# Performance work log

Measured on AMD Instinct MI355X. Metric: run time of the kernel, lower is better.

## Reference

```python
import jax, jax.numpy as jnp
import numpy as np

MODES = 32
NUM_BLOCKS = 4
NUM_EXPERTS = 16
TOP_K = 4
TEMPERATURE = 2.0


def _gelu(t):
    return jax.nn.gelu(t, approximate=False)  # torch F.gelu default (erf)


def _c1(x, w, b):
    # 1x1 conv: x [B,C,H,W], w [O,C], b [O]
    return jnp.einsum('bchw,oc->bohw', x, w) + b[None, :, None, None]


def _group_norm(x, w, b, groups=8, eps=1e-5):
    B, C, H, W = x.shape
    xg = x.reshape(B, groups, C // groups, H, W)
    mu = xg.mean(axis=(2, 3, 4), keepdims=True)
    var = xg.var(axis=(2, 3, 4), keepdims=True)
    xn = ((xg - mu) * jax.lax.rsqrt(var + eps)).reshape(B, C, H, W)
    return xn * w[None, :, None, None] + b[None, :, None, None]


def _bn_eval(x, g, b, rm, rv, eps=1e-5):
    # eval-mode BatchNorm with running stats
    return (x - rm) * jax.lax.rsqrt(rv + eps) * g + b


def _afno(x, w1, b1, w2, b2):
    # x: [B,C,H,W] (channel_first). Block-diagonal complex MLP on low FFT modes.
    B, C, H, W = x.shape
    bs = C // NUM_BLOCKS
    xp = x.transpose(0, 2, 3, 1)                      # [B,H,W,C]
    xf = jnp.fft.rfft2(xp, axes=(1, 2), norm='ortho') # [B,H,Wf,C] complex64
    Wf = xf.shape[2]
    xf = xf.reshape(B, H, Wf, NUM_BLOCKS, bs)
    m = MODES
    xm = xf[:, :m, :m]                                # kept modes only
    xr, xi = xm.real, xm.imag
    o1r = _gelu(jnp.einsum('bhwni,nio->bhwno', xr, w1[0])
                - jnp.einsum('bhwni,nio->bhwno', xi, w1[1]) + b1[0])
    o1i = _gelu(jnp.einsum('bhwni,nio->bhwno', xi, w1[0])
                + jnp.einsum('bhwni,nio->bhwno', xr, w1[1]) + b1[1])
    o2r = (jnp.einsum('bhwni,nio->bhwno', o1r, w2[0])
           - jnp.einsum('bhwni,nio->bhwno', o1i, w2[1]) + b2[0])
    o2i = (jnp.einsum('bhwni,nio->bhwno', o1i, w2[0])
           + jnp.einsum('bhwni,nio->bhwno', o1r, w2[1]) + b2[1])
    of = jnp.zeros((B, H, Wf, NUM_BLOCKS, bs), dtype=xf.dtype)
    of = of.at[:, :m, :m].set(o2r + 1j * o2i)
    out = jnp.fft.irfft2(of.reshape(B, H, Wf, C), s=(H, W), axes=(1, 2), norm='ortho')
    out = out + xp
    return out.transpose(0, 3, 1, 2)


def _forward(x, gn1_w, gn1_b, afno_w1, afno_b1, afno_w2, afno_b2,
             gn2_w, gn2_b, fe_w, fe_b, g1_w, g1_b, bn1_g, bn1_b, bn1_rm, bn1_rv,
             ca_w1, ca_b1, ca_w2, ca_b2, g2_w, g2_b, bn2_g, bn2_b, bn2_rm, bn2_rv,
             g3_w, g3_b, shared_w, shared_b, expert_w, expert_b):
    residual = x
    h = _group_norm(x, gn1_w, gn1_b)
    h = _afno(h, afno_w1, afno_b1, afno_w2, afno_b2)
    h = h + residual            # double_skip
    residual = h
    h = _group_norm(h, gn2_w, gn2_b)
    # MoEImage (eval mode -> loss_gate = 0)
    feats = _gelu(_c1(h, fe_w, fe_b))
    shared = jnp.zeros_like(h)
    for s in range(shared_w.shape[0]):
        shared = shared + _gelu(_c1(feats, shared_w[s], shared_b[s])) / shared_w.shape[0]
    # gating on global-avg-pooled features (1x1 convs == linears)
    gf = feats.mean(axis=(2, 3))                              # [B,C]
    h1 = _gelu(_bn_eval(gf @ g1_w.T + g1_b, bn1_g, bn1_b, bn1_rm, bn1_rv))
    a = _gelu(h1 @ ca_w1.T + ca_b1) @ ca_w2.T + ca_b2
    h1 = h1 * jax.nn.sigmoid(2.0 * a)                          # avg==max pool on 1x1 map
    h2 = _gelu(_bn_eval(h1 @ g2_w.T + g2_b, bn2_g, bn2_b, bn2_rm, bn2_rv))
    scores = h2 @ g3_w.T + g3_b                                # [B,E]
    vals, idx = jax.lax.top_k(scores, TOP_K)
    wts = jax.nn.softmax(vals / TEMPERATURE, axis=1)
    B = x.shape[0]
    gate_w = jnp.zeros((B, NUM_EXPERTS), x.dtype).at[jnp.arange(B)[:, None], idx].add(wts)
    out = shared
    for e in range(NUM_EXPERTS):
        out = out + _gelu(_c1(feats, expert_w[e], expert_b[e])) * gate_w[:, e][:, None, None, None]
    return out + residual


def setup_inputs():
    key = jax.random.key(0)
    ks = jax.random.split(key, 16)
    B, C, H, W = 8, 64, 192, 192
    nb = NUM_BLOCKS
    bs = C // nb
    E = NUM_EXPERTS
    scale = 1.0 / (bs * bs)
    f32 = jnp.float32
    n = lambda k, shape: jax.random.normal(k, shape, f32) * 0.02
    return {
        'x': jax.random.normal(ks[0], (B, C, H, W), f32),
        'gn1_w': jnp.ones((C,), f32), 'gn1_b': jnp.zeros((C,), f32),
        'afno_w1': jax.random.uniform(ks[1], (2, nb, bs, bs), f32) * scale,
        'afno_b1': jax.random.uniform(ks[2], (2, nb, bs), f32) * scale,
        'afno_w2': jax.random.uniform(ks[3], (2, nb, bs, bs), f32) * scale,
        'afno_b2': jax.random.uniform(ks[4], (2, nb, bs), f32) * scale,
        'gn2_w': jnp.ones((C,), f32), 'gn2_b': jnp.zeros((C,), f32),
        'fe_w': n(ks[5], (C, C)), 'fe_b': jnp.zeros((C,), f32),
        'g1_w': n(ks[6], (2 * C, C)), 'g1_b': jnp.zeros((2 * C,), f32),
        'bn1_g': jnp.ones((2 * C,), f32), 'bn1_b': jnp.zeros((2 * C,), f32),
        'bn1_rm': jnp.zeros((2 * C,), f32), 'bn1_rv': jnp.ones((2 * C,), f32),
        'ca_w1': n(ks[7], (2 * C // 16, 2 * C)), 'ca_b1': jnp.zeros((2 * C // 16,), f32),
        'ca_w2': n(ks[8], (2 * C, 2 * C // 16)), 'ca_b2': jnp.zeros((2 * C,), f32),
        'g2_w': n(ks[9], (C, 2 * C)), 'g2_b': jnp.zeros((C,), f32),
        'bn2_g': jnp.ones((C,), f32), 'bn2_b': jnp.zeros((C,), f32),
        'bn2_rm': jnp.zeros((C,), f32), 'bn2_rv': jnp.ones((C,), f32),
        'g3_w': n(ks[10], (E, C)), 'g3_b': jnp.zeros((E,), f32),
        'shared_w': n(ks[11], (2, C, C)), 'shared_b': jnp.zeros((2, C), f32),
        'expert_w': n(ks[12], (E, C, C)), 'expert_b': jnp.zeros((E, C), f32),
    }


def reference(x, gn1_w, gn1_b, afno_w1, afno_b1, afno_w2, afno_b2,
              gn2_w, gn2_b, fe_w, fe_b, g1_w, g1_b, bn1_g, bn1_b, bn1_rm, bn1_rv,
              ca_w1, ca_b1, ca_w2, ca_b2, g2_w, g2_b, bn2_g, bn2_b, bn2_rm, bn2_rv,
              g3_w, g3_b, shared_w, shared_b, expert_w, expert_b):
    return _forward(x, gn1_w, gn1_b, afno_w1, afno_b1, afno_w2, afno_b2,
                    gn2_w, gn2_b, fe_w, fe_b, g1_w, g1_b, bn1_g, bn1_b, bn1_rm, bn1_rv,
                    ca_w1, ca_b1, ca_w2, ca_b2, g2_w, g2_b, bn2_g, bn2_b, bn2_rm, bn2_rv,
                    g3_w, g3_b, shared_w, shared_b, expert_w, expert_b)
```

## Files before the change

kernel.cpp:

```cpp
#include <hip/hip_runtime.h>
#include <math.h>

#define TPI 6.283185307179586f

typedef __attribute__((ext_vector_type(8))) short bf8v;
typedef __attribute__((ext_vector_type(4))) float f4v;

#define MFMA(a,b,c) __builtin_amdgcn_mfma_f32_16x16x32_bf16((a),(b),(c),0,0,0)

__device__ __forceinline__ float gelu_f(float v){
  return 0.5f*v*(1.0f+erff(v*0.7071067811865475f));
}
__device__ __forceinline__ float gelu_fast(float x){
  float x2=x*x;
  float inner=fmaf(0.044715f*x2, x, x);
  float e=__expf(1.5957691216057308f*inner);
  float r=__builtin_amdgcn_rcpf(1.0f+e);
  return fmaf(-x, r, x);
}
__device__ __forceinline__ float gelu_sig(float x){
  float e=__expf(-1.702f*x);
  return x*__builtin_amdgcn_rcpf(1.0f+e);
}
__device__ __forceinline__ unsigned short f2b(float f){
  union{float f; unsigned u;} v; v.f=f;
  unsigned r=v.u + 0x7FFFu + ((v.u>>16)&1u);
  return (unsigned short)(r>>16);
}

__global__ __launch_bounds__(256) void prep(const float* __restrict__ shw, const float* __restrict__ exw,
    const float* __restrict__ shb, const float* __restrict__ exb, const float* __restrict__ few,
    unsigned short* __restrict__ T, unsigned short* __restrict__ wall, float* __restrict__ ball,
    unsigned short* __restrict__ wfe, float* __restrict__ gfp){
  const float a = TPI/192.0f;
  int stride=gridDim.x*256;
  for(int i=blockIdx.x*256+threadIdx.x; i<61440; i+=stride){
    float v;
    if(i<12288){
      int n1=i/192, w=i%192; int kw=n1>>1, c=n1&1;
      int m=(kw*w)%192; float cs,sn; sincosf((float)m*a,&sn,&cs);
      v = c ? -sn : cs;
    } else if(i<36864){
      int j=i-12288; int n1=j/384, k1=j%384; int kh=n1>>1, d=n1&1; int h=k1>>1, c=k1&1;
      int m=(kh*h)%192; float cs,sn; sincosf((float)m*a,&sn,&cs);
      float e = d ? (c ? cs : -sn) : (c ? sn : cs);
      v = e*(1.0f/192.0f);
    } else if(i<49152){
      int j=i-36864; int h=j/64, k1=j%64; int kh=k1>>1, c=k1&1;
      int m=(h*kh)%192; float cs,sn; sincosf((float)m*a,&sn,&cs);
      v = c ? sn : cs;
    } else {
      int j=i-49152; int w=j/64, k1=j%64; int kw=k1>>1, d=k1&1;
      float f = kw ? (2.0f/192.0f) : (1.0f/192.0f);
      int m=(w*kw)%192; float cs,sn; sincosf((float)m*a,&sn,&cs);
      v = d ? -f*sn : f*cs;
    }
    T[i]=f2b(v);
  }
  for(int i=blockIdx.x*256+threadIdx.x;i<73728;i+=stride) wall[i]=f2b(i<8192?shw[i]:exw[i-8192]);
  for(int i=blockIdx.x*256+threadIdx.x;i<1152;i+=stride)  ball[i]=(i<128)?shb[i]:exb[i-128];
  for(int i=blockIdx.x*256+threadIdx.x;i<4096;i+=stride)  wfe[i]=f2b(few[i]);
  for(int i=blockIdx.x*256+threadIdx.x;i<512;i+=stride)   gfp[i]=0.f;
}

__global__ void gn_finalize(const float* __restrict__ part, const float* __restrict__ gw,
                            const float* __restrict__ gb, float2* __restrict__ sb){
  int g=threadIdx.x; if(g>=64) return;
  float S=0,SS=0;
  for(int j=0;j<8;j++){ S+=part[(g*8+j)*2]; SS+=part[(g*8+j)*2+1]; }
  const float inv=1.0f/294912.0f;
  float mean=S*inv, var=SS*inv-mean*mean;
  float rstd=rsqrtf(var+1e-5f);
  int b=g>>3, gg=g&7;
  for(int k=0;k<8;k++){
    int c=gg*8+k;
    float sc=rstd*gw[c];
    sb[b*64+c]=make_float2(sc, gb[c]-mean*sc);
  }
}

__global__ __launch_bounds__(256) void fwd_dft(const float* __restrict__ x,
      const unsigned short* __restrict__ TBf1, const unsigned short* __restrict__ TBf2,
      float* __restrict__ Xm2, float* __restrict__ part1){
  __shared__ __align__(16) unsigned short ldsA[64*200];
  __shared__ __align__(16) float sX[2048];
  __shared__ float red[8];
  int t=threadIdx.x, bc=blockIdx.x;
  int wave=t>>6, l=t&63, lr=l&15, lg=l>>4;
  const float* xch = x + (size_t)bc*36864;
  for(int i=t;i<1536;i+=256){
    int row=i/24, chunk=i%24;
    *(uint4*)&ldsA[row*200 + chunk*8] = *(const uint4*)(TBf1 + row*192 + chunk*8);
  }
  __syncthreads();
  float s_=0.f, ss_=0.f;
  f4v acc1[3][4];
  for(int mt=0;mt<3;mt++){
    int m0=(wave+mt*4)*16;
    const float* xrow = xch + (m0+lr)*192 + lg*8;
    bf8v af[6];
    #pragma unroll
    for(int ks=0;ks<6;ks++){
      float4 u0=*(const float4*)(xrow+ks*32);
      float4 u1=*(const float4*)(xrow+ks*32+4);
      s_ += u0.x+u0.y+u0.z+u0.w+u1.x+u1.y+u1.z+u1.w;
      ss_+= u0.x*u0.x+u0.y*u0.y+u0.z*u0.z+u0.w*u0.w
           +u1.x*u1.x+u1.y*u1.y+u1.z*u1.z+u1.w*u1.w;
      bf8v a;
      a[0]=(short)f2b(u0.x); a[1]=(short)f2b(u0.y); a[2]=(short)f2b(u0.z); a[3]=(short)f2b(u0.w);
      a[4]=(short)f2b(u1.x); a[5]=(short)f2b(u1.y); a[6]=(short)f2b(u1.z); a[7]=(short)f2b(u1.w);
      af[ks]=a;
    }
    #pragma unroll
    for(int nt=0;nt<4;nt++){
      f4v acc={0.f,0.f,0.f,0.f};
      #pragma unroll
      for(int ks=0;ks<6;ks++){
        bf8v b=*(const bf8v*)&ldsA[(nt*16+lr)*200 + ks*32 + lg*8];
        acc=MFMA(af[ks],b,acc);
      }
      acc1[mt][nt]=acc;
    }
  }
  __syncthreads();
  for(int mt=0;mt<3;mt++){
    int m0=(wave+mt*4)*16;
    #pragma unroll
    for(int nt=0;nt<4;nt++){
      int n1=nt*16+lr; int kw=n1>>1, c=n1&1;
      #pragma unroll
      for(int reg=0;reg<4;reg++){
        int h=m0+4*lg+reg;
        ldsA[kw*392 + 2*h + c]=f2b(acc1[mt][nt][reg]);
      }
    }
  }
  __syncthreads();
  for(int pp=0;pp<2;pp++){
    int p=wave+pp*4;
    int m0=(p>>2)*16, n0=(p&3)*16;
    f4v acc={0.f,0.f,0.f,0.f};
    #pragma unroll
    for(int ks=0;ks<12;ks++){
      bf8v a=*(const bf8v*)&ldsA[(m0+lr)*392 + ks*32 + lg*8];
      bf8v b=*(const bf8v*)(TBf2 + (n0+lr)*384 + ks*32 + lg*8);
      acc=MFMA(a,b,acc);
    }
    int n1=n0+lr; int kh=n1>>1, d=n1&1;
    #pragma unroll
    for(int reg=0;reg<4;reg++){
      int kw=m0+4*lg+reg;
      sX[(kh*32+kw)*2 + d]=acc[reg];
    }
  }
  __syncthreads();
  float* dst=Xm2+(size_t)bc*2048;
  for(int i=t;i<512;i+=256) *(float4*)(dst+i*4)=*(const float4*)(sX+i*4);
  #pragma unroll
  for(int o=32;o>0;o>>=1){ s_+=__shfl_down(s_,o); ss_+=__shfl_down(ss_,o); }
  if(l==0){ red[wave]=s_; red[4+wave]=ss_; }
  __syncthreads();
  if(t==0){
    part1[bc*2]  =red[0]+red[1]+red[2]+red[3];
    part1[bc*2+1]=red[4]+red[5]+red[6]+red[7];
  }
}

__global__ __launch_bounds__(256) void mode_mlp(const float* __restrict__ Xm2, const float2* __restrict__ sb1,
    const float* __restrict__ w1, const float* __restrict__ b1,
    const float* __restrict__ w2, const float* __restrict__ b2,
    float* __restrict__ S2){
  __shared__ float w10[1024], w11[1024], w20[1024], w21[1024];
  __shared__ float b10[64], b11[64], b20[64], b21[64];
  __shared__ float2 sbl[64];
  __shared__ float xr[32][64], xi[32][64];
  __shared__ float o1r[32][64], o1i[32][64];
  int t=threadIdx.x;
  int b=blockIdx.x>>5, kh=blockIdx.x&31;
  for(int i=t;i<1024;i+=256){ w10[i]=w1[i]; w11[i]=w1[1024+i]; w20[i]=w2[i]; w21[i]=w2[1024+i]; }
  if(t<64){ b10[t]=b1[t]; b11[t]=b1[64+t]; b20[t]=b2[t]; b21[t]=b2[64+t]; sbl[t]=sb1[b*64+t]; }
  __syncthreads();
  for(int q=0;q<16;q++){
    int idx=q*256+t; int c=idx>>6, jj=idx&63;
    float2 s=sbl[c];
    float v=Xm2[((size_t)(b*64+c))*2048 + kh*64 + jj]*s.x;
    if(kh==0 && jj==0) v += 192.0f*s.y;
    if(jj&1) xi[jj>>1][c]=v; else xr[jj>>1][c]=v;
  }
  __syncthreads();
  int tl=t&63, n=tl>>4, o=tl&15, wb=n*256+o;
  #pragma unroll
  for(int it=0;it<8;it++){
    int kw=(t>>6)+it*4;
    float a_r=b10[tl], a_i=b11[tl];
    #pragma unroll
    for(int i=0;i<16;i++){
      float rr=xr[kw][n*16+i], im=xi[kw][n*16+i];
      float W0=w10[wb+i*16], W1=w11[wb+i*16];
      a_r=fmaf(rr,W0,fmaf(-im,W1,a_r));
      a_i=fmaf(im,W0,fmaf( rr,W1,a_i));
    }
    o1r[kw][tl]=gelu_f(a_r); o1i[kw][tl]=gelu_f(a_i);
  }
  __syncthreads();
  #pragma unroll
  for(int it=0;it<8;it++){
    int kw=(t>>6)+it*4;
    float c_r=b20[tl], c_i=b21[tl];
    #pragma unroll
    for(int i=0;i<16;i++){
      float rr=o1r[kw][n*16+i], im=o1i[kw][n*16+i];
      float W0=w20[wb+i*16], W1=w21[wb+i*16];
      c_r=fmaf(rr,W0,fmaf(-im,W1,c_r));
      c_i=fmaf(im,W0,fmaf( rr,W1,c_i));
    }
    xr[kw][tl]=c_r; xi[kw][tl]=c_i;
  }
  __syncthreads();
  for(int q=0;q<16;q++){
    int idx=q*256+t; int c=idx>>6, jj=idx&63;
    float v = (jj&1) ? xi[jj>>1][c] : xr[jj>>1][c];
    S2[((size_t)(b*64+c))*2048 + kh*64 + jj]=v;
  }
}

__global__ __launch_bounds__(256) void inv_dft(const float* __restrict__ S2,
      const unsigned short* __restrict__ TAi, const unsigned short* __restrict__ TBi,
      const float* __restrict__ x, const float2* __restrict__ sb,
      float* __restrict__ h2, float* __restrict__ part2){
  __shared__ __align__(16) unsigned short Bs[64*72];
  __shared__ __align__(16) unsigned short GL[192*72];
  __shared__ float red[8];
  int t=threadIdx.x, bc=blockIdx.x;
  int wave=t>>6, l=t&63, lr=l&15, lg=l>>4;
  const float* sp=S2+(size_t)bc*2048;
  for(int i=t;i<1024;i+=256){
    int kh=i>>5, kw=i&31;
    float Sr=sp[(kh*32+kw)*2], Si=sp[(kh*32+kw)*2+1];
    unsigned short br=f2b(Sr), bi_=f2b(Si), nbi=f2b(-Si);
    Bs[(2*kw+0)*72 + 2*kh+0]=br;
    Bs[(2*kw+0)*72 + 2*kh+1]=nbi;
    Bs[(2*kw+1)*72 + 2*kh+0]=bi_;
    Bs[(2*kw+1)*72 + 2*kh+1]=br;
  }
  __syncthreads();
  for(int mt=0;mt<3;mt++){
    int m0=(wave+mt*4)*16;
    bf8v a0=*(const bf8v*)(TAi + (m0+lr)*64 + lg*8);
    bf8v a1=*(const bf8v*)(TAi + (m0+lr)*64 + 32 + lg*8);
    #pragma unroll
    for(int nt=0;nt<4;nt++){
      f4v acc={0.f,0.f,0.f,0.f};
      bf8v b0=*(const bf8v*)&Bs[(nt*16+lr)*72 + lg*8];
      bf8v b1=*(const bf8v*)&Bs[(nt*16+lr)*72 + 32 + lg*8];
      acc=MFMA(a0,b0,acc); acc=MFMA(a1,b1,acc);
      #pragma unroll
      for(int reg=0;reg<4;reg++)
        GL[(m0+4*lg+reg)*72 + nt*16+lr]=f2b(acc[reg]);
    }
  }
  __syncthreads();
  float2 sv=sb[bc];
  float cA=sv.x+1.0f, cB=sv.y;
  asm volatile("" : "+v"(cA), "+v"(cB));
  const float* xch=x+(size_t)bc*36864;
  float* och=h2+(size_t)bc*36864;
  float s_=0.f, ss_=0.f;
  for(int mt=0;mt<3;mt++){
    int m0=(wave+mt*4)*16;
    bf8v a0=*(const bf8v*)&GL[(m0+lr)*72 + lg*8];
    bf8v a1=*(const bf8v*)&GL[(m0+lr)*72 + 32 + lg*8];
    for(int nt=0;nt<12;nt++){
      int n0=nt*16;
      f4v acc={0.f,0.f,0.f,0.f};
      bf8v b0=*(const bf8v*)(TBi + (n0+lr)*64 + lg*8);
      bf8v b1=*(const bf8v*)(TBi + (n0+lr)*64 + 32 + lg*8);
      acc=MFMA(a0,b0,acc); acc=MFMA(a1,b1,acc);
      int w=n0+lr;
      #pragma unroll
      for(int reg=0;reg<4;reg++){
        int h=m0+4*lg+reg;
        int ga=h*192+w;
        float xv=xch[ga];
        float val=acc[reg]+fmaf(cA,xv,cB);
        och[ga]=val;
        s_+=val; ss_+=val*val;
      }
    }
  }
  #pragma unroll
  for(int o=32;o>0;o>>=1){ s_+=__shfl_down(s_,o); ss_+=__shfl_down(ss_,o); }
  if(l==0){ red[wave]=s_; red[4+wave]=ss_; }
  __syncthreads();
  if(t==0){
    part2[bc*2]  =red[0]+red[1]+red[2]+red[3];
    part2[bc*2+1]=red[4]+red[5]+red[6]+red[7];
  }
}

__global__ __launch_bounds__(256,4) void gf_k(const float* __restrict__ h2, const float2* __restrict__ sb,
    const unsigned short* __restrict__ wfe, const float* __restrict__ feb,
    float* __restrict__ gfp, unsigned short* __restrict__ feats){
  __shared__ __align__(16) unsigned short A[128*72];
  __shared__ float sgf[64];
  int t=threadIdx.x;
  int blk=blockIdx.x, b=blk/288, tile=blk-b*288, hw0=tile*128;
  if(t<64) sgf[t]=0.f;
  float4 v[8];
  #pragma unroll
  for(int k=0;k<8;k++){
    int i=t+k*256; int c=i>>5, q=i&31;
    v[k]=*(const float4*)&h2[(size_t)(b*64+c)*36864 + hw0 + q*4];
  }
  #pragma unroll
  for(int k=0;k<8;k++){
    int i=t+k*256; int c=i>>5, q=i&31;
    float2 s=sb[b*64+c];
    int px0=q*4, sw=((px0>>4)&3)<<3, cc=c^sw;
    A[(px0+0)*72+cc]=f2b(fmaf(v[k].x,s.x,s.y));
    A[(px0+1)*72+cc]=f2b(fmaf(v[k].y,s.x,s.y));
    A[(px0+2)*72+cc]=f2b(fmaf(v[k].z,s.x,s.y));
    A[(px0+3)*72+cc]=f2b(fmaf(v[k].w,s.x,s.y));
  }
  __syncthreads();
  int wave=t>>6, l=t&63, lr=l&15, lg=l>>4;
  int pxb=wave*32;
  bf8v af[2][2];
  #pragma unroll
  for(int fm=0;fm<2;fm++){
    int row=pxb+fm*16+lr, sw=((row>>4)&3)<<3;
    #pragma unroll
    for(int ks=0;ks<2;ks++) af[fm][ks]=*(const bf8v*)&A[row*72+((ks*32+lg*8)^sw)];
  }
  float gsum[4]={0.f,0.f,0.f,0.f};
  #pragma unroll
  for(int fn=0;fn<4;fn++){
    bf8v b0=*(const bf8v*)(wfe+(fn*16+lr)*64+lg*8);
    bf8v b1=*(const bf8v*)(wfe+(fn*16+lr)*64+32+lg*8);
    float bs=feb[fn*16+lr];
    #pragma unroll
    for(int fm=0;fm<2;fm++){
      f4v acc={0.f,0.f,0.f,0.f};
      acc=MFMA(af[fm][0],b0,acc);
      acc=MFMA(af[fm][1],b1,acc);
      int swm=(((pxb+fm*16)>>4)&3)<<3;
      int cc=(fn*16+lr)^swm;
      #pragma unroll
      for(int r=0;r<4;r++){
        float g=gelu_fast(acc[r]+bs);
        gsum[fn]+=g;
        A[(pxb+fm*16+4*lg+r)*72+cc]=f2b(g);
      }
    }
  }
  #pragma unroll
  for(int fn=0;fn<4;fn++){
    float v2=gsum[fn];
    v2+=__shfl_xor(v2,16); v2+=__shfl_xor(v2,32);
    if(lg==0) atomicAdd(&sgf[fn*16+lr], v2);
  }
  __syncthreads();
  if(t<64) atomicAdd(&gfp[b*64+t], sgf[t]);
  #pragma unroll
  for(int k=0;k<4;k++){
    int i=t+k*256; int px=i>>3, c0=(i&7)*8, sw=((px>>4)&3)<<3;
    *(uint4*)&feats[(size_t)(b*36864+hw0+px)*64+c0] = *(const uint4*)&A[px*72+(c0^sw)];
  }
}

__global__ __launch_bounds__(128) void gating(const float* __restrict__ gfp,
  const float* __restrict__ g1w, const float* __restrict__ g1b,
  const float* __restrict__ bn1g, const float* __restrict__ bn1b, const float* __restrict__ bn1m, const float* __restrict__ bn1v,
  const float* __restrict__ cw1, const float* __restrict__ cb1, const float* __restrict__ cw2, const float* __restrict__ cb2,
  const float* __restrict__ g2w, const float* __restrict__ g2b,
  const float* __restrict__ bn2g, const float* __restrict__ bn2b, const float* __restrict__ bn2m, const float* __restrict__ bn2v,
  const float* __restrict__ g3w, const float* __restrict__ g3b, float2* __restrict__ act){
  __shared__ float gf[8][64];
  __shared__ float h1[8][128];
  __shared__ float a1[8][8];
  __shared__ float h2g[8][64];
  __shared__ float sc[8][16];
  int t=threadIdx.x;
  for(int i=t;i<512;i+=128) gf[i>>6][i&63]=gfp[i]*(1.0f/36864.0f);
  __syncthreads();
  for(int i=t;i<1024;i+=128){
    int b=i>>7, j=i&127;
    float s=g1b[j];
    for(int c=0;c<64;c++) s=fmaf(gf[b][c], g1w[j*64+c], s);
    s=(s-bn1m[j])*rsqrtf(bn1v[j]+1e-5f)*bn1g[j]+bn1b[j];
    h1[b][j]=gelu_f(s);
  }
  __syncthreads();
  if(t<64){
    int b=t>>3, k=t&7; float s=cb1[k];
    for(int j=0;j<128;j++) s=fmaf(h1[b][j], cw1[k*128+j], s);
    a1[b][k]=gelu_f(s);
  }
  __syncthreads();
  for(int i=t;i<1024;i+=128){
    int b=i>>7, j=i&127;
    float s=cb2[j];
    for(int k=0;k<8;k++) s=fmaf(a1[b][k], cw2[j*8+k], s);
    h1[b][j]=h1[b][j]/(1.0f+expf(-2.0f*s));
  }
  __syncthreads();
  for(int i=t;i<512;i+=128){
    int b=i>>6, j=i&63;
    float s=g2b[j];
    for(int k=0;k<128;k++) s=fmaf(h1[b][k], g2w[j*128+k], s);
    s=(s-bn2m[j])*rsqrtf(bn2v[j]+1e-5f)*bn2g[j]+bn2b[j];
    h2g[b][j]=gelu_f(s);
  }
  __syncthreads();
  {
    int b=t>>4, e=t&15;
    float s=g3b[e];
    for(int c=0;c<64;c++) s=fmaf(h2g[b][c], g3w[e*64+c], s);
    sc[b][e]=s;
  }
  __syncthreads();
  if(t<8){
    int b=t;
    float v[16];
    for(int e=0;e<16;e++) v[e]=sc[b][e];
    float vals[4]; int idx[4];
    for(int k=0;k<4;k++){
      float best=-1e30f; int bi=0;
      for(int e=0;e<16;e++) if(v[e]>best){best=v[e];bi=e;}
      vals[k]=best; idx[k]=bi; v[bi]=-1e30f;
    }
    float m=vals[0], ssum=0.f, w[4];
    for(int k=0;k<4;k++){ w[k]=expf((vals[k]-m)*0.5f); ssum+=w[k]; }
    act[b*6+0]=make_float2(0.5f, __int_as_float(0));
    act[b*6+1]=make_float2(0.5f, __int_as_float(1));
    for(int k=0;k<4;k++) act[b*6+2+k]=make_float2(w[k]/ssum, __int_as_float(2+idx[k]));
  }
}

__global__ __launch_bounds__(256,4) void final_k(const unsigned short* __restrict__ feats,
  const float* __restrict__ h2w,
  const unsigned short* __restrict__ wall, const float* __restrict__ ball,
  const float2* __restrict__ act, float* __restrict__ out){
  __shared__ __align__(16) float Fo[32*132];
  int t=threadIdx.x;
  int blk=blockIdx.x, b=blk/288, tile=blk-b*288, hw0=tile*128;
  int wave=t>>6, l=t&63, lr=l&15, lg=l>>4;
  int pxb=wave*32;
  float gv[6]; int tv[6];
  #pragma unroll
  for(int j=0;j<6;j++){
    float2 aw=act[b*6+j];
    gv[j]=aw.x; tv[j]=__float_as_int(aw.y);
  }
  const unsigned short* fbase = feats + (size_t)(b*36864+hw0)*64;
  bf8v af2[2][2];
  #pragma unroll
  for(int fm=0;fm<2;fm++){
    int row=pxb+fm*16+lr;
    #pragma unroll
    for(int ks=0;ks<2;ks++)
      af2[fm][ks]=*(const bf8v*)(fbase + (size_t)row*64 + ks*32 + lg*8);
  }
  #pragma unroll
  for(int half=0;half<2;half++){
    float oa[2][2][4]={};
    #pragma unroll
    for(int j=0;j<6;j++){
      float g=gv[j];
      const unsigned short* wp=wall+tv[j]*4096;
      const float* bp=ball+tv[j]*64;
      #pragma unroll
      for(int fn2=0;fn2<2;fn2++){
        int fn=half*2+fn2;
        bf8v b0=*(const bf8v*)(wp+(fn*16+lr)*64+lg*8);
        bf8v b1=*(const bf8v*)(wp+(fn*16+lr)*64+32+lg*8);
        float bs=bp[fn*16+lr];
        #pragma unroll
        for(int fm=0;fm<2;fm++){
          f4v acc={0.f,0.f,0.f,0.f};
          acc=MFMA(af2[fm][0],b0,acc);
          acc=MFMA(af2[fm][1],b1,acc);
          #pragma unroll
          for(int r=0;r<4;r++)
            oa[fm][fn2][r]=fmaf(g, gelu_sig(acc[r]+bs), oa[fm][fn2][r]);
        }
      }
    }
    __syncthreads();
    #pragma unroll
    for(int fm=0;fm<2;fm++)
      #pragma unroll
      for(int fn2=0;fn2<2;fn2++){
        int ocl=fn2*16+lr;
        *(float4*)&Fo[ocl*132 + pxb + fm*16 + 4*lg] =
            make_float4(oa[fm][fn2][0],oa[fm][fn2][1],oa[fm][fn2][2],oa[fm][fn2][3]);
      }
    __syncthreads();
    for(int i=t;i<1024;i+=256){
      int ocl=i>>5, px0=(i&31)*4;
      int oc=half*32+ocl;
      size_t base=(size_t)(b*64+oc)*36864 + hw0 + px0;
      float4 rv=*(const float4*)&h2w[base];
      float4 ov=*(const float4*)&Fo[ocl*132+px0];
      *(float4*)&out[base]=make_float4(ov.x+rv.x,ov.y+rv.y,ov.z+rv.z,ov.w+rv.w);
    }
  }
}

extern "C" void kernel_launch(void* const* d_in, const int* in_sizes, int n_in,
                              void* d_out, int out_size, void* d_ws, size_t ws_size,
                              hipStream_t stream){
  const float* x    =(const float*)d_in[0];
  const float* gn1w =(const float*)d_in[1];
  const float* gn1b =(const float*)d_in[2];
  const float* aw1  =(const float*)d_in[3];
  const float* ab1  =(const float*)d_in[4];
  const float* aw2  =(const float*)d_in[5];
  const float* ab2  =(const float*)d_in[6];
  const float* gn2w =(const float*)d_in[7];
  const float* gn2b =(const float*)d_in[8];
  const float* few  =(const float*)d_in[9];
  const float* feb  =(const float*)d_in[10];
  const float* g1w  =(const float*)d_in[11];
  const float* g1b  =(const float*)d_in[12];
  const float* bn1g =(const float*)d_in[13];
  const float* bn1b =(const float*)d_in[14];
  const float* bn1m =(const float*)d_in[15];
  const float* bn1v =(const float*)d_in[16];
  const float* cw1  =(const float*)d_in[17];
  const float* cb1  =(const float*)d_in[18];
  const float* cw2  =(const float*)d_in[19];
  const float* cb2  =(const float*)d_in[20];
  const float* g2w  =(const float*)d_in[21];
  const float* g2b  =(const float*)d_in[22];
  const float* bn2g =(const float*)d_in[23];
  const float* bn2b =(const float*)d_in[24];
  const float* bn2m =(const float*)d_in[25];
  const float* bn2v =(const float*)d_in[26];
  const float* g3w  =(const float*)d_in[27];
  const float* g3b  =(const float*)d_in[28];
  const float* shw  =(const float*)d_in[29];
  const float* shb  =(const float*)d_in[30];
  const float* exw  =(const float*)d_in[31];
  const float* exb  =(const float*)d_in[32];

  float* out=(float*)d_out;
  float* ws=(float*)d_ws;

  float*  part1 = ws;
  float*  part2 = ws+1024;
  float2* sb1   = (float2*)(ws+2048);
  float2* sb2   = (float2*)(ws+3072);
  float2* act   = (float2*)(ws+4096);
  float*  gfp   = ws+4224;
  float*  Xm2   = ws+8192;
  float*  S2    = ws+1056768;
  unsigned short* Tbl  = (unsigned short*)(ws+2105344);
  unsigned short* wall = (unsigned short*)(ws+2136064);
  float*          ball = ws+2172928;
  unsigned short* wfe  = (unsigned short*)(ws+2174080);
  unsigned short* feats= (unsigned short*)(ws+2176128);
  float*  h2w   = ws+11613312;
  const unsigned short* TBf1 = Tbl;
  const unsigned short* TBf2 = Tbl+12288;
  const unsigned short* TAi  = Tbl+36864;
  const unsigned short* TBi  = Tbl+49152;

  prep<<<64,256,0,stream>>>(shw, exw, shb, exb, few, Tbl, wall, ball, wfe, gfp);
  fwd_dft <<<512,256,0,stream>>>(x, TBf1, TBf2, Xm2, part1);
  gn_finalize<<<1,64,0,stream>>>(part1, gn1w, gn1b, sb1);
  mode_mlp<<<256,256,0,stream>>>(Xm2, sb1, aw1, ab1, aw2, ab2, S2);
  inv_dft <<<512,256,0,stream>>>(S2, TAi, TBi, x, sb1, h2w, part2);
  gn_finalize<<<1,64,0,stream>>>(part2, gn2w, gn2b, sb2);
  gf_k<<<2304,256,0,stream>>>(h2w, sb2, wfe, feb, gfp, feats);
  gating <<<1,128,0,stream>>>(gfp, g1w,g1b, bn1g,bn1b,bn1m,bn1v,
                              cw1,cb1,cw2,cb2, g2w,g2b, bn2g,bn2b,bn2m,bn2v,
                              g3w,g3b, act);
  final_k<<<2304,256,0,stream>>>(feats, h2w, wall, ball, act, out);
}
```

Before: 211.2 us.

## Store intermediate h2 in bf16 and write final output directly from registers

The AFNO output h2 is now stored as bf16 instead of fp32. That halves its write traffic in inv_dft and its read traffic in gf_k and final_k. final_k also drops its shared-memory staging tile and two barriers, adding the residual and writing float4 output straight from the MFMA accumulators. The cost is lower precision on the residual path added to the output, and less coalesced 16-byte stores in final_k.

```diff
diff --git a/kernel.cpp b/kernel.cpp
--- a/kernel.cpp
+++ b/kernel.cpp
@@ -26,6 +26,9 @@
   union{float f; unsigned u;} v; v.f=f;
   unsigned r=v.u + 0x7FFFu + ((v.u>>16)&1u);
   return (unsigned short)(r>>16);
+}
+__device__ __forceinline__ float b2f(unsigned short h){
+  union{unsigned u; float f;} v; v.u=((unsigned)h)<<16; return v.f;
 }
 
 __global__ __launch_bounds__(256) void prep(const float* __restrict__ shw, const float* __restrict__ exw,
@@ -227,7 +230,7 @@
 __global__ __launch_bounds__(256) void inv_dft(const float* __restrict__ S2,
       const unsigned short* __restrict__ TAi, const unsigned short* __restrict__ TBi,
       const float* __restrict__ x, const float2* __restrict__ sb,
-      float* __restrict__ h2, float* __restrict__ part2){
+      unsigned short* __restrict__ h2b, float* __restrict__ part2){
   __shared__ __align__(16) unsigned short Bs[64*72];
   __shared__ __align__(16) unsigned short GL[192*72];
   __shared__ float red[8];
@@ -264,7 +267,7 @@
   float cA=sv.x+1.0f, cB=sv.y;
   asm volatile("" : "+v"(cA), "+v"(cB));
   const float* xch=x+(size_t)bc*36864;
-  float* och=h2+(size_t)bc*36864;
+  unsigned short* och=h2b+(size_t)bc*36864;
   float s_=0.f, ss_=0.f;
   for(int mt=0;mt<3;mt++){
     int m0=(wave+mt*4)*16;
@@ -283,7 +286,7 @@
         int ga=h*192+w;
         float xv=xch[ga];
         float val=acc[reg]+fmaf(cA,xv,cB);
-        och[ga]=val;
+        och[ga]=f2b(val);
         s_+=val; ss_+=val*val;
       }
     }
@@ -298,7 +301,7 @@
   }
 }
 
-__global__ __launch_bounds__(256,4) void gf_k(const float* __restrict__ h2, const float2* __restrict__ sb,
+__global__ __launch_bounds__(256,4) void gf_k(const unsigned short* __restrict__ h2b, const float2* __restrict__ sb,
     const unsigned short* __restrict__ wfe, const float* __restrict__ feb,
     float* __restrict__ gfp, unsigned short* __restrict__ feats){
   __shared__ __align__(16) unsigned short A[128*72];
@@ -306,21 +309,21 @@
   int t=threadIdx.x;
   int blk=blockIdx.x, b=blk/288, tile=blk-b*288, hw0=tile*128;
   if(t<64) sgf[t]=0.f;
-  float4 v[8];
-  #pragma unroll
-  for(int k=0;k<8;k++){
-    int i=t+k*256; int c=i>>5, q=i&31;
-    v[k]=*(const float4*)&h2[(size_t)(b*64+c)*36864 + hw0 + q*4];
-  }
-  #pragma unroll
-  for(int k=0;k<8;k++){
-    int i=t+k*256; int c=i>>5, q=i&31;
+  uint4 v[4];
+  #pragma unroll
+  for(int k=0;k<4;k++){
+    int i=t+k*256; int c=i>>4, o=i&15;
+    v[k]=*(const uint4*)&h2b[(size_t)(b*64+c)*36864 + hw0 + o*8];
+  }
+  #pragma unroll
+  for(int k=0;k<4;k++){
+    int i=t+k*256; int c=i>>4, o=i&15;
     float2 s=sb[b*64+c];
-    int px0=q*4, sw=((px0>>4)&3)<<3, cc=c^sw;
-    A[(px0+0)*72+cc]=f2b(fmaf(v[k].x,s.x,s.y));
-    A[(px0+1)*72+cc]=f2b(fmaf(v[k].y,s.x,s.y));
-    A[(px0+2)*72+cc]=f2b(fmaf(v[k].z,s.x,s.y));
-    A[(px0+3)*72+cc]=f2b(fmaf(v[k].w,s.x,s.y));
+    int sw=((o>>1)&3)<<3, cc=c^sw;
+    const unsigned short* pv=(const unsigned short*)&v[k];
+    #pragma unroll
+    for(int r=0;r<8;r++)
+      A[(o*8+r)*72+cc]=f2b(fmaf(b2f(pv[r]),s.x,s.y));
   }
   __syncthreads();
   int wave=t>>6, l=t&63, lr=l&15, lg=l>>4;
@@ -438,10 +441,9 @@
 }
 
 __global__ __launch_bounds__(256,4) void final_k(const unsigned short* __restrict__ feats,
-  const float* __restrict__ h2w,
+  const unsigned short* __restrict__ h2b,
   const unsigned short* __restrict__ wall, const float* __restrict__ ball,
   const float2* __restrict__ act, float* __restrict__ out){
-  __shared__ __align__(16) float Fo[32*132];
   int t=threadIdx.x;
   int blk=blockIdx.x, b=blk/288, tile=blk-b*288, hw0=tile*128;
   int wave=t>>6, l=t&63, lr=l&15, lg=l>>4;
@@ -486,24 +488,20 @@
         }
       }
     }
-    __syncthreads();
     #pragma unroll
     for(int fm=0;fm<2;fm++)
       #pragma unroll
       for(int fn2=0;fn2<2;fn2++){
-        int ocl=fn2*16+lr;
-        *(float4*)&Fo[ocl*132 + pxb + fm*16 + 4*lg] =
-            make_float4(oa[fm][fn2][0],oa[fm][fn2][1],oa[fm][fn2][2],oa[fm][fn2][3]);
+        int oc=half*32+fn2*16+lr;
+        int px=pxb+fm*16+4*lg;
+        size_t base=(size_t)(b*64+oc)*36864 + hw0 + px;
+        ushort4 hv=*(const ushort4*)&h2b[base];
+        float4 o=make_float4(oa[fm][fn2][0]+b2f(hv.x),
+                             oa[fm][fn2][1]+b2f(hv.y),
+                             oa[fm][fn2][2]+b2f(hv.z),
+                             oa[fm][fn2][3]+b2f(hv.w));
+        *(float4*)&out[base]=o;
       }
-    __syncthreads();
-    for(int i=t;i<1024;i+=256){
-      int ocl=i>>5, px0=(i&31)*4;
-      int oc=half*32+ocl;
-      size_t base=(size_t)(b*64+oc)*36864 + hw0 + px0;
-      float4 rv=*(const float4*)&h2w[base];
-      float4 ov=*(const float4*)&Fo[ocl*132+px0];
-      *(float4*)&out[base]=make_float4(ov.x+rv.x,ov.y+rv.y,ov.z+rv.z,ov.w+rv.w);
-    }
   }
 }
 
@@ -560,7 +558,7 @@
   float*          ball = ws+2172928;
   unsigned short* wfe  = (unsigned short*)(ws+2174080);
   unsigned short* feats= (unsigned short*)(ws+2176128);
-  float*  h2w   = ws+11613312;
+  unsigned short* h2b  = (unsigned short*)(ws+11613312);
   const unsigned short* TBf1 = Tbl;
   const unsigned short* TBf2 = Tbl+12288;
   const unsigned short* TAi  = Tbl+36864;
@@ -570,11 +568,11 @@
   fwd_dft <<<512,256,0,stream>>>(x, TBf1, TBf2, Xm2, part1);
   gn_finalize<<<1,64,0,stream>>>(part1, gn1w, gn1b, sb1);
   mode_mlp<<<256,256,0,stream>>>(Xm2, sb1, aw1, ab1, aw2, ab2, S2);
-  inv_dft <<<512,256,0,stream>>>(S2, TAi, TBi, x, sb1, h2w, part2);
+  inv_dft <<<512,256,0,stream>>>(S2, TAi, TBi, x, sb1, h2b, part2);
   gn_finalize<<<1,64,0,stream>>>(part2, gn2w, gn2b, sb2);
-  gf_k<<<2304,256,0,stream>>>(h2w, sb2, wfe, feb, gfp, feats);
+  gf_k<<<2304,256,0,stream>>>(h2b, sb2, wfe, feb, gfp, feats);
   gating <<<1,128,0,stream>>>(gfp, g1w,g1b, bn1g,bn1b,bn1m,bn1v,
                               cw1,cb1,cw2,cb2, g2w,g2b, bn2g,bn2b,bn2m,bn2v,
                               g3w,g3b, act);
-  final_k<<<2304,256,0,stream>>>(feats, h2w, wall, ball, act, out);
-}
+  final_k<<<2304,256,0,stream>>>(feats, h2b, wall, ball, act, out);
+}
```

After: 227.3 us. +7.6%, slower.
